# Kernel tuning notes

Hardware: AMD Instinct MI355X
Metric: run time of the kernel (lower is better)

The kernel has to match this reference:

```python
import jax, jax.numpy as jnp
import numpy as np

RADIUS = 4  # matches init radius


def _bilinear_sample(v, grid):
    """Faithful F.grid_sample(v, grid, mode='bilinear', align_corners=True, padding_mode='zeros').
    v: (B,C,H,W); grid: (B,Hg,Wg,2) in [-1,1]; grid[...,0]->width(x), grid[...,1]->height(y)."""
    B, C, H, W = v.shape
    Hg, Wg = grid.shape[1], grid.shape[2]
    ix = (grid[..., 0] + 1.0) * 0.5 * (W - 1)
    iy = (grid[..., 1] + 1.0) * 0.5 * (H - 1)
    x0 = jnp.floor(ix); y0 = jnp.floor(iy)
    x1 = x0 + 1.0;      y1 = y0 + 1.0
    wx1 = ix - x0; wx0 = 1.0 - wx1
    wy1 = iy - y0; wy0 = 1.0 - wy1
    v_flat = v.reshape(B, C, H * W)
    out = jnp.zeros((B, C, Hg, Wg), v.dtype)
    for xf, yf, w in ((x0, y0, wx0 * wy0), (x1, y0, wx1 * wy0),
                      (x0, y1, wx0 * wy1), (x1, y1, wx1 * wy1)):
        valid = (xf >= 0) & (xf <= W - 1) & (yf >= 0) & (yf <= H - 1)
        xi = jnp.clip(xf, 0, W - 1).astype(jnp.int32)
        yi = jnp.clip(yf, 0, H - 1).astype(jnp.int32)
        idx = (yi * W + xi).reshape(B, 1, Hg * Wg)
        g = jnp.take_along_axis(v_flat, idx, axis=2).reshape(B, C, Hg, Wg)
        out = out + g * (w * valid)[:, None, :, :]
    return out


def setup_inputs() -> dict:
    key = jax.random.key(0)
    ks = jax.random.split(key, 5)
    B, C, H, W, K = 4, 128, 128, 128, 8
    x = jax.random.normal(ks[0], (B, C, H, W), jnp.float32)
    psf_tbl = jax.random.randint(ks[1], (B, H, W, K, 2), 0, 128)  # absolute pixel anchors
    delta = jax.random.normal(ks[2], (1, 1, 1, K, 2), jnp.float32) * 0.1
    w_qkv = jax.random.normal(ks[3], (3 * C, C), jnp.float32) * (C ** -0.5)  # 1x1 conv, no bias
    w_proj = jax.random.normal(ks[4], (C, C), jnp.float32) * (C ** -0.5)
    return {"x": x, "psf_tbl": psf_tbl, "delta": delta, "w_qkv": w_qkv, "w_proj": w_proj}


def reference(x, psf_tbl, delta, w_qkv, w_proj):
    B, C, H, W = x.shape
    K = psf_tbl.shape[3]
    qkv = jnp.einsum('oc,bchw->bohw', w_qkv, x)  # 1x1 conv to_qkv
    q, k, v = jnp.split(qkv, 3, axis=1)
    offsets = psf_tbl.astype(x.dtype) + jnp.tanh(delta) * RADIUS  # (B,H,W,K,2)
    norm = jnp.array([H - 1, W - 1], x.dtype)
    grid = (offsets / norm * 2.0 - 1.0).reshape(B, H, W * K, 2)
    k_s = _bilinear_sample(k, grid).reshape(B, C, H, W, K)
    v_s = _bilinear_sample(v, grid).reshape(B, C, H, W, K)
    attn = jnp.einsum('bchw,bchwk->bhwk', q, k_s) * (C ** -0.5)
    attn = jax.nn.softmax(attn, axis=-1)  # softmax over K sampled points
    out = jnp.einsum('bhwk,bchwk->bchw', attn, v_s)
    return x + jnp.einsum('oc,bchw->bohw', w_proj, out)
```

## Files before the change

kernel.cpp:

```cpp
#include <hip/hip_runtime.h>

#define HW 16384
#define C 128

typedef __attribute__((ext_vector_type(8))) short short8;
typedef __attribute__((ext_vector_type(4))) float f32x4;
typedef __attribute__((ext_vector_type(2))) float f32x2;
typedef __attribute__((ext_vector_type(16))) int v16i;

__device__ __forceinline__ unsigned short f2bf(float f) {
  union { float f; unsigned u; } v; v.f = f;
  return (unsigned short)((v.u + 0x7fffu + ((v.u >> 16) & 1u)) >> 16);
}
#if __has_builtin(__builtin_amdgcn_cvt_pk_bf16_f32)
typedef __attribute__((ext_vector_type(2))) __bf16 bf16x2;
__device__ __forceinline__ unsigned pk2(float a, float b) {
  union { bf16x2 v; unsigned u; } cv;
  cv.v = __builtin_amdgcn_cvt_pk_bf16_f32(a, b);
  return cv.u;
}
#else
__device__ __forceinline__ unsigned pk2(float a, float b) {
  return (unsigned)f2bf(a) | ((unsigned)f2bf(b) << 16);
}
#endif
__device__ __forceinline__ unsigned short f2bf1(float a) {
  return (unsigned short)(pk2(a, a) & 0xffffu);
}
__device__ __forceinline__ float bflo(unsigned w) {
  union { unsigned u; float f; } v; v.u = w << 16; return v.f;
}
__device__ __forceinline__ float bfhi(unsigned w) {
  union { unsigned u; float f; } v; v.u = w & 0xffff0000u; return v.f;
}
__device__ __forceinline__ float asf(int u) {
  union { int u; float f; } v; v.u = u; return v.f;
}
__device__ __forceinline__ float bf2f(unsigned short h) {
  union { unsigned u; float f; } v; v.u = ((unsigned)h) << 16; return v.f;
}

__global__ __launch_bounds__(128) void k_prep(const float* __restrict__ w_qkv,
                                              const float* __restrict__ w_proj,
                                              const float* __restrict__ delta,
                                              unsigned short* __restrict__ Mt,
                                              unsigned short* __restrict__ Pm,
                                              float* __restrict__ pw,
                                              int* __restrict__ pi) {
  const int bid = blockIdx.x;
  const int t = threadIdx.x;
  if (bid == 256) {
    if (t < 8) {
      float s0 = tanhf(delta[t * 2 + 0]) * 4.0f;
      float s1 = tanhf(delta[t * 2 + 1]) * 4.0f;
      float f0 = floorf(s0), f1 = floorf(s1);
      pi[2 * t + 0] = (int)f0;
      pi[2 * t + 1] = (int)f1;
      float fx = s0 - f0, fy = s1 - f1;
      pw[4 * t + 0] = (1.0f - fx) * (1.0f - fy);
      pw[4 * t + 1] = fx * (1.0f - fy);
      pw[4 * t + 2] = (1.0f - fx) * fy;
      pw[4 * t + 3] = fx * fy;
    }
    return;
  }
  const int R = bid & 127;
  float acc = 0.0f;
  if (bid < 128) {
    const float* wq = w_qkv;
    const float* wk = w_qkv + 128 * 128;
    #pragma unroll 16
    for (int j = 0; j < 128; ++j)
      acc += wk[j * 128 + R] * wq[j * 128 + t];
    acc *= 0.08838834764831845f;
    Mt[R * 128 + (t ^ ((R & 7) << 3))] = f2bf1(acc);
  } else {
    const float* wv = w_qkv + 2 * 128 * 128;
    const float* wp = w_proj + (size_t)R * 128;
    #pragma unroll 16
    for (int j = 0; j < 128; ++j)
      acc += wp[j] * wv[j * 128 + t];
    Pm[R * 128 + (t ^ ((R & 7) << 3))] = f2bf1(acc);
  }
}

__global__ __launch_bounds__(256) void k_qx(const float* __restrict__ x,
                                            const unsigned short* __restrict__ Mt,
                                            unsigned short* __restrict__ qb,
                                            unsigned* __restrict__ xq) {
  __shared__ __align__(16) unsigned short Xs[128 * 128];
  const int t = threadIdx.x;
  const int gpix0 = blockIdx.x * 128;
  const int b = gpix0 >> 14;
  const int hw0 = gpix0 & (HW - 1);

  const float* xb = x + (size_t)b * C * HW + hw0;
  #pragma unroll
  for (int i = 0; i < 16; ++i) {
    int linear = i * 256 + t;
    int p = linear & 127;
    int c4 = (linear >> 7) * 4;
    float a0 = xb[(size_t)(c4 + 0) * HW + p];
    float a1 = xb[(size_t)(c4 + 1) * HW + p];
    float a2 = xb[(size_t)(c4 + 2) * HW + p];
    float a3 = xb[(size_t)(c4 + 3) * HW + p];
    int cc = c4 ^ ((p & 7) << 3);
    *(uint2*)&Xs[p * 128 + cc] = make_uint2(pk2(a0, a1), pk2(a2, a3));
  }
  __syncthreads();

  #pragma unroll
  for (int i = 0; i < 8; ++i) {
    int linear = i * 256 + t;
    int c8 = (linear & 15) * 8;
    int prow = linear >> 4;
    uint4 v = *(const uint4*)&Xs[prow * 128 + (c8 ^ ((prow & 7) << 3))];
    *(uint4*)&xq[((size_t)(gpix0 + prow)) * 64 + (c8 >> 1)] = v;
  }

  const int wave = t >> 6, lane = t & 63;
  const int wr = wave >> 1, wc = wave & 1;
  const int rsel = lane & 15, quad = lane >> 4;

  f32x4 acc[4][4];
  #pragma unroll
  for (int mi = 0; mi < 4; ++mi)
    #pragma unroll
    for (int ni = 0; ni < 4; ++ni) acc[mi][ni] = (f32x4){0.f, 0.f, 0.f, 0.f};
  #pragma unroll
  for (int ks = 0; ks < 4; ++ks) {
    const int koff = ks * 32 + quad * 8;
    short8 afr[4], bfr[4];
    #pragma unroll
    for (int mi = 0; mi < 4; ++mi) {
      int r = wr * 64 + mi * 16 + rsel;
      afr[mi] = *(const short8*)&Xs[r * 128 + (koff ^ ((r & 7) << 3))];
    }
    #pragma unroll
    for (int ni = 0; ni < 4; ++ni) {
      int r = wc * 64 + ni * 16 + rsel;
      bfr[ni] = *(const short8*)&Mt[r * 128 + (koff ^ ((r & 7) << 3))];
    }
    #pragma unroll
    for (int mi = 0; mi < 4; ++mi)
      #pragma unroll
      for (int ni = 0; ni < 4; ++ni)
        acc[mi][ni] = __builtin_amdgcn_mfma_f32_16x16x32_bf16(afr[mi], bfr[ni], acc[mi][ni], 0, 0, 0);
  }
  __syncthreads();
  #pragma unroll
  for (int mi = 0; mi < 4; ++mi)
    #pragma unroll
    for (int ni = 0; ni < 4; ++ni)
      #pragma unroll
      for (int r = 0; r < 4; ++r) {
        int p = wr * 64 + mi * 16 + quad * 4 + r;
        int ch = wc * 64 + ni * 16 + rsel;
        Xs[p * 128 + (ch ^ ((p & 7) << 3))] = f2bf1(acc[mi][ni][r]);
      }
  __syncthreads();
  #pragma unroll
  for (int i = 0; i < 8; ++i) {
    int linear = i * 256 + t;
    int c8 = (linear & 15) * 8;
    int prow = linear >> 4;
    uint4 v = *(const uint4*)&Xs[prow * 128 + (c8 ^ ((prow & 7) << 3))];
    *(uint4*)(qb + (size_t)(gpix0 + prow) * C + c8) = v;
  }
}

__global__ __launch_bounds__(256) void k_attn(const unsigned short* __restrict__ qb,
                                              const unsigned* __restrict__ xq,
                                              const int* __restrict__ psf,
                                              const int* __restrict__ pwu,
                                              unsigned short* __restrict__ ao) {
  const int t = threadIdx.x;
  const int li = t & 31;
  const int half = (t >> 5) & 1;
  const int gid = blockIdx.x;
  const int b = gid & 3;
  const int grp = gid >> 2;
  const int pixl = (grp << 3) + ((t >> 6) << 1) + half;
  const size_t spix = ((size_t)b << 14) + pixl;

  v16i w0, w1, tpi;
  asm volatile(
      "s_load_dwordx16 %0, %3, 0\n\t"
      "s_load_dwordx16 %1, %3, 64\n\t"
      "s_load_dwordx16 %2, %3, 128\n\t"
      "s_waitcnt lgkmcnt(0)"
      : "=&s"(w0), "=&s"(w1), "=&s"(tpi)
      : "s"(pwu));

  const int4* pr = (const int4*)(psf + spix * 16);
  int4 a0 = pr[0], a1 = pr[1], a2 = pr[2], a3 = pr[3];
  int va[16] = {a0.x, a0.y, a0.z, a0.w, a1.x, a1.y, a1.z, a1.w,
                a2.x, a2.y, a2.z, a2.w, a3.x, a3.y, a3.z, a3.w};

  const uint2 qp = *(const uint2*)((const unsigned*)qb + spix * 64 + 2 * li);
  const float q0 = bflo(qp.x), q1 = bfhi(qp.x);
  const float q2 = bflo(qp.y), q3 = bfhi(qp.y);

  const unsigned* xB = xq + (((size_t)b << 14) << 6);

  float s0[8], s1[8], s2[8], s3[8], dk[8];
  #pragma unroll
  for (int k = 0; k < 8; ++k) {
    const int x0 = va[2 * k + 0] + tpi[2 * k + 0];
    const int y0 = va[2 * k + 1] + tpi[2 * k + 1];
    float t0 = 0.f, t1 = 0.f, t2 = 0.f, t3 = 0.f;
    #pragma unroll
    for (int cn = 0; cn < 4; ++cn) {
      const int xi = x0 + (cn & 1);
      const int yi = y0 + (cn >> 1);
      const bool valid = ((unsigned)xi <= 127u) & ((unsigned)yi <= 127u);
      const int xc = min(max(xi, 0), 127);
      const int yc = min(max(yi, 0), 127);
      const int widx = k * 4 + cn;
      const float wv = valid ? asf(widx < 16 ? w0[widx & 15] : w1[widx & 15]) : 0.0f;
      const uint2 w2 = *(const uint2*)&xB[((size_t)((yc << 7) + xc) << 6) + 2 * li];
      t0 = fmaf(bflo(w2.x), wv, t0); t1 = fmaf(bfhi(w2.x), wv, t1);
      t2 = fmaf(bflo(w2.y), wv, t2); t3 = fmaf(bfhi(w2.y), wv, t3);
    }
    s0[k] = t0; s1[k] = t1; s2[k] = t2; s3[k] = t3;
    dk[k] = fmaf(q0, t0, fmaf(q1, t1, fmaf(q2, t2, q3 * t3)));
  }
  #pragma unroll
  for (int off = 16; off > 0; off >>= 1) {
    #pragma unroll
    for (int k = 0; k < 8; ++k) dk[k] += __shfl_xor(dk[k], off);
  }
  float m = dk[0];
  #pragma unroll
  for (int k = 1; k < 8; ++k) m = fmaxf(m, dk[k]);
  float den = 0.0f;
  #pragma unroll
  for (int k = 0; k < 8; ++k) { dk[k] = __expf(dk[k] - m); den += dk[k]; }
  const float inv = 1.0f / den;
  float o0 = 0.f, o1 = 0.f, o2 = 0.f, o3 = 0.f;
  #pragma unroll
  for (int k = 0; k < 8; ++k) {
    const float pk = dk[k] * inv;
    o0 = fmaf(pk, s0[k], o0); o1 = fmaf(pk, s1[k], o1);
    o2 = fmaf(pk, s2[k], o2); o3 = fmaf(pk, s3[k], o3);
  }
  *(uint2*)((unsigned*)ao + spix * 64 + 2 * li) = make_uint2(pk2(o0, o1), pk2(o2, o3));
}

__global__ __launch_bounds__(256) void k_proj(const unsigned short* __restrict__ ao,
                                              const unsigned short* __restrict__ Pm,
                                              const unsigned short* __restrict__ xqh,
                                              float* __restrict__ out) {
  __shared__ __align__(16) unsigned short As[128 * 128];
  const int t = threadIdx.x;
  const int gpix0 = blockIdx.x * 128;
  const int b = gpix0 >> 14;
  const int hw0 = gpix0 & (HW - 1);

  #pragma unroll
  for (int i = 0; i < 8; ++i) {
    int linear = i * 256 + t;
    int c8 = (linear & 15) * 8;
    int p = linear >> 4;
    uint4 v = *(const uint4*)(ao + (size_t)(gpix0 + p) * C + c8);
    *(uint4*)&As[p * 128 + (c8 ^ ((p & 7) << 3))] = v;
  }
  __syncthreads();

  const int wave = t >> 6, lane = t & 63;
  const int wr = wave >> 1, wc = wave & 1;
  const int rsel = lane & 15, quad = lane >> 4;

  f32x4 acc[4][4];
  #pragma unroll
  for (int mi = 0; mi < 4; ++mi)
    #pragma unroll
    for (int ni = 0; ni < 4; ++ni) acc[mi][ni] = (f32x4){0.f, 0.f, 0.f, 0.f};

  #pragma unroll
  for (int ks = 0; ks < 4; ++ks) {
    const int koff = ks * 32 + quad * 8;
    short8 afr[4], bfr[4];
    #pragma unroll
    for (int mi = 0; mi < 4; ++mi) {
      int r = wr * 64 + mi * 16 + rsel;
      afr[mi] = *(const short8*)&Pm[r * 128 + (koff ^ ((r & 7) << 3))];
    }
    #pragma unroll
    for (int ni = 0; ni < 4; ++ni) {
      int r = wc * 64 + ni * 16 + rsel;
      bfr[ni] = *(const short8*)&As[r * 128 + (koff ^ ((r & 7) << 3))];
    }
    #pragma unroll
    for (int mi = 0; mi < 4; ++mi)
      #pragma unroll
      for (int ni = 0; ni < 4; ++ni)
        acc[mi][ni] = __builtin_amdgcn_mfma_f32_16x16x32_bf16(afr[mi], bfr[ni], acc[mi][ni], 0, 0, 0);
  }

  __syncthreads();
  #pragma unroll
  for (int i = 0; i < 8; ++i) {
    int linear = i * 256 + t;
    int c8 = (linear & 15) * 8;
    int p = linear >> 4;
    uint4 v = *(const uint4*)(xqh + (size_t)(gpix0 + p) * C + c8);
    *(uint4*)&As[p * 128 + (c8 ^ ((p & 7) << 3))] = v;
  }
  __syncthreads();

  #pragma unroll
  for (int mi = 0; mi < 4; ++mi)
    #pragma unroll
    for (int ni = 0; ni < 4; ++ni)
      #pragma unroll
      for (int r = 0; r < 4; ++r) {
        int och = wr * 64 + mi * 16 + quad * 4 + r;
        int pixl = wc * 64 + ni * 16 + rsel;
        float xr = bf2f(As[pixl * 128 + (och ^ ((pixl & 7) << 3))]);
        size_t addr = ((size_t)b * C + och) * HW + hw0 + pixl;
        out[addr] = xr + acc[mi][ni][r];
      }
}

extern "C" void kernel_launch(void* const* d_in, const int* in_sizes, int n_in,
                              void* d_out, int out_size, void* d_ws, size_t ws_size,
                              hipStream_t stream) {
  const float* x      = (const float*)d_in[0];
  const int*   psf    = (const int*)d_in[1];
  const float* delta  = (const float*)d_in[2];
  const float* w_qkv  = (const float*)d_in[3];
  const float* w_proj = (const float*)d_in[4];
  float* out = (float*)d_out;

  const size_t N = (size_t)4 * HW * C;
  unsigned short* qb = (unsigned short*)d_ws;
  unsigned short* xq = qb + N;
  unsigned short* ao = xq + N;
  unsigned short* Mt = ao + N;
  unsigned short* Pm = Mt + 16384;
  float* pw = (float*)(Pm + 16384);
  int*   pi = (int*)(pw + 32);
  (void)pi;

  k_prep<<<dim3(257), 128, 0, stream>>>(w_qkv, w_proj, delta, Mt, Pm, pw, pi);
  k_qx<<<dim3(512), 256, 0, stream>>>(x, Mt, qb, (unsigned*)xq);
  k_attn<<<dim3(8192), 256, 0, stream>>>(qb, (const unsigned*)xq, psf, (const int*)pw, ao);
  k_proj<<<dim3(512), 256, 0, stream>>>(ao, Pm, xq, out);
}
```

Baseline: 149.6 us.

## Split x transpose/convert from q GEMM into separate kernels with more blocks

The fused k_qx kernel is split in two. k_xq converts and transposes x into the bf16 pixel-major buffer using 2048 small blocks with float4 loads. k_q then reads that buffer back and runs the q GEMM. The aim is more parallelism and better coalescing for the memory-bound transpose, at the cost of an extra launch and a re-read of xq. The gather offset in k_attn is also switched to 32-bit unsigned arithmetic to cut address computation.

```diff
diff --git a/kernel.cpp b/kernel.cpp
--- a/kernel.cpp
+++ b/kernel.cpp
@@ -84,39 +84,54 @@
   }
 }
 
-__global__ __launch_bounds__(256) void k_qx(const float* __restrict__ x,
-                                            const unsigned short* __restrict__ Mt,
-                                            unsigned short* __restrict__ qb,
+__global__ __launch_bounds__(256) void k_xq(const float* __restrict__ x,
                                             unsigned* __restrict__ xq) {
-  __shared__ __align__(16) unsigned short Xs[128 * 128];
-  const int t = threadIdx.x;
-  const int gpix0 = blockIdx.x * 128;
+  __shared__ __align__(16) unsigned short Xs[32 * 128];
+  const int t = threadIdx.x;
+  const int gpix0 = blockIdx.x * 32;
   const int b = gpix0 >> 14;
   const int hw0 = gpix0 & (HW - 1);
-
   const float* xb = x + (size_t)b * C * HW + hw0;
-  #pragma unroll
-  for (int i = 0; i < 16; ++i) {
-    int linear = i * 256 + t;
-    int p = linear & 127;
-    int c4 = (linear >> 7) * 4;
-    float a0 = xb[(size_t)(c4 + 0) * HW + p];
-    float a1 = xb[(size_t)(c4 + 1) * HW + p];
-    float a2 = xb[(size_t)(c4 + 2) * HW + p];
-    float a3 = xb[(size_t)(c4 + 3) * HW + p];
-    int cc = c4 ^ ((p & 7) << 3);
-    *(uint2*)&Xs[p * 128 + cc] = make_uint2(pk2(a0, a1), pk2(a2, a3));
-  }
-  __syncthreads();
+
+  #pragma unroll
+  for (int i = 0; i < 4; ++i) {
+    int idx = i * 256 + t;
+    int c = idx >> 3;
+    int p4 = idx & 7;
+    float4 v = *(const float4*)(xb + (size_t)c * HW + p4 * 4);
+    int p0 = p4 * 4;
+    Xs[(p0 + 0) * 128 + (c ^ (((p0 + 0) & 7) << 3))] = f2bf1(v.x);
+    Xs[(p0 + 1) * 128 + (c ^ (((p0 + 1) & 7) << 3))] = f2bf1(v.y);
+    Xs[(p0 + 2) * 128 + (c ^ (((p0 + 2) & 7) << 3))] = f2bf1(v.z);
+    Xs[(p0 + 3) * 128 + (c ^ (((p0 + 3) & 7) << 3))] = f2bf1(v.w);
+  }
+  __syncthreads();
+  #pragma unroll
+  for (int i = 0; i < 2; ++i) {
+    int idx = i * 256 + t;
+    int pix = idx >> 4;
+    int c8 = (idx & 15) * 8;
+    uint4 v = *(const uint4*)&Xs[pix * 128 + (c8 ^ ((pix & 7) << 3))];
+    *(uint4*)&xq[(size_t)(gpix0 + pix) * 64 + (c8 >> 1)] = v;
+  }
+}
+
+__global__ __launch_bounds__(256) void k_q(const unsigned short* __restrict__ xqh,
+                                           const unsigned short* __restrict__ Mt,
+                                           unsigned short* __restrict__ qb) {
+  __shared__ __align__(16) unsigned short Xs[128 * 128];
+  const int t = threadIdx.x;
+  const int gpix0 = blockIdx.x * 128;
 
   #pragma unroll
   for (int i = 0; i < 8; ++i) {
     int linear = i * 256 + t;
     int c8 = (linear & 15) * 8;
-    int prow = linear >> 4;
-    uint4 v = *(const uint4*)&Xs[prow * 128 + (c8 ^ ((prow & 7) << 3))];
-    *(uint4*)&xq[((size_t)(gpix0 + prow)) * 64 + (c8 >> 1)] = v;
-  }
+    int p = linear >> 4;
+    uint4 v = *(const uint4*)(xqh + (size_t)(gpix0 + p) * C + c8);
+    *(uint4*)&Xs[p * 128 + (c8 ^ ((p & 7) << 3))] = v;
+  }
+  __syncthreads();
 
   const int wave = t >> 6, lane = t & 63;
   const int wr = wave >> 1, wc = wave & 1;
@@ -218,7 +233,8 @@
       const int yc = min(max(yi, 0), 127);
       const int widx = k * 4 + cn;
       const float wv = valid ? asf(widx < 16 ? w0[widx & 15] : w1[widx & 15]) : 0.0f;
-      const uint2 w2 = *(const uint2*)&xB[((size_t)((yc << 7) + xc) << 6) + 2 * li];
+      const unsigned off = (((unsigned)((yc << 7) + xc)) << 6) + 2u * (unsigned)li;
+      const uint2 w2 = *(const uint2*)&xB[off];
       t0 = fmaf(bflo(w2.x), wv, t0); t1 = fmaf(bfhi(w2.x), wv, t1);
       t2 = fmaf(bflo(w2.y), wv, t2); t3 = fmaf(bfhi(w2.y), wv, t3);
     }
@@ -344,7 +360,8 @@
   (void)pi;
 
   k_prep<<<dim3(257), 128, 0, stream>>>(w_qkv, w_proj, delta, Mt, Pm, pw, pi);
-  k_qx<<<dim3(512), 256, 0, stream>>>(x, Mt, qb, (unsigned*)xq);
+  k_xq<<<dim3(2048), 256, 0, stream>>>(x, (unsigned*)xq);
+  k_q<<<dim3(512), 256, 0, stream>>>(xq, Mt, qb);
   k_attn<<<dim3(8192), 256, 0, stream>>>(qb, (const unsigned*)xq, psf, (const int*)pw, ao);
   k_proj<<<dim3(512), 256, 0, stream>>>(ao, Pm, xq, out);
 }
```

After: 155.9 us. 4.2% more time.

## Fuse output projection and residual add into attention kernel

Applied to the files above, without the earlier changes.

Folds the separate projection GEMM kernel into the attention kernel. Each 8-pixel block stages its bf16 attention output in LDS, padded to 16 rows, and runs a small MFMA against the projection weights. It then adds the fp32 residual from x and writes the result directly. This removes the ao round-trip through global memory and one kernel launch. In exchange, each block reads the whole 32KB Pm matrix for only 8 pixels, half the MFMA work is wasted on padding, and the output stores are only 8 floats contiguous per channel row. The gather address math is also narrowed to 32-bit offsets.

```diff
diff --git a/kernel.cpp b/kernel.cpp
--- a/kernel.cpp
+++ b/kernel.cpp
@@ -35,9 +35,6 @@
 }
 __device__ __forceinline__ float asf(int u) {
   union { int u; float f; } v; v.u = u; return v.f;
-}
-__device__ __forceinline__ float bf2f(unsigned short h) {
-  union { unsigned u; float f; } v; v.u = ((unsigned)h) << 16; return v.f;
 }
 
 __global__ __launch_bounds__(128) void k_prep(const float* __restrict__ w_qkv,
@@ -173,15 +170,22 @@
                                               const unsigned* __restrict__ xq,
                                               const int* __restrict__ psf,
                                               const int* __restrict__ pwu,
-                                              unsigned short* __restrict__ ao) {
+                                              const unsigned short* __restrict__ Pm,
+                                              const float* __restrict__ x,
+                                              float* __restrict__ out) {
+  __shared__ __align__(16) unsigned short Ot[16 * 128];
   const int t = threadIdx.x;
   const int li = t & 31;
   const int half = (t >> 5) & 1;
+  const int wave = t >> 6;
   const int gid = blockIdx.x;
   const int b = gid & 3;
   const int grp = gid >> 2;
-  const int pixl = (grp << 3) + ((t >> 6) << 1) + half;
+  const int p0 = grp << 3;
+  const int pixl = p0 + (wave << 1) + half;
   const size_t spix = ((size_t)b << 14) + pixl;
+
+  ((uint2*)(Ot + 8 * 128))[t] = make_uint2(0u, 0u);
 
   v16i w0, w1, tpi;
   asm volatile(
@@ -218,7 +222,8 @@
       const int yc = min(max(yi, 0), 127);
       const int widx = k * 4 + cn;
       const float wv = valid ? asf(widx < 16 ? w0[widx & 15] : w1[widx & 15]) : 0.0f;
-      const uint2 w2 = *(const uint2*)&xB[((size_t)((yc << 7) + xc) << 6) + 2 * li];
+      const unsigned off = (((unsigned)((yc << 7) + xc)) << 6) + 2u * (unsigned)li;
+      const uint2 w2 = *(const uint2*)&xB[off];
       t0 = fmaf(bflo(w2.x), wv, t0); t1 = fmaf(bfhi(w2.x), wv, t1);
       t2 = fmaf(bflo(w2.y), wv, t2); t3 = fmaf(bfhi(w2.y), wv, t3);
     }
@@ -244,83 +249,38 @@
     o0 = fmaf(pk, s0[k], o0); o1 = fmaf(pk, s1[k], o1);
     o2 = fmaf(pk, s2[k], o2); o3 = fmaf(pk, s3[k], o3);
   }
-  *(uint2*)((unsigned*)ao + spix * 64 + 2 * li) = make_uint2(pk2(o0, o1), pk2(o2, o3));
-}
-
-__global__ __launch_bounds__(256) void k_proj(const unsigned short* __restrict__ ao,
-                                              const unsigned short* __restrict__ Pm,
-                                              const unsigned short* __restrict__ xqh,
-                                              float* __restrict__ out) {
-  __shared__ __align__(16) unsigned short As[128 * 128];
-  const int t = threadIdx.x;
-  const int gpix0 = blockIdx.x * 128;
-  const int b = gpix0 >> 14;
-  const int hw0 = gpix0 & (HW - 1);
-
-  #pragma unroll
-  for (int i = 0; i < 8; ++i) {
-    int linear = i * 256 + t;
-    int c8 = (linear & 15) * 8;
-    int p = linear >> 4;
-    uint4 v = *(const uint4*)(ao + (size_t)(gpix0 + p) * C + c8);
-    *(uint4*)&As[p * 128 + (c8 ^ ((p & 7) << 3))] = v;
-  }
+  const int prow = (wave << 1) + half;
+  *(uint2*)&Ot[prow * 128 + ((4 * li) ^ ((prow & 7) << 3))] =
+      make_uint2(pk2(o0, o1), pk2(o2, o3));
   __syncthreads();
 
-  const int wave = t >> 6, lane = t & 63;
-  const int wr = wave >> 1, wc = wave & 1;
-  const int rsel = lane & 15, quad = lane >> 4;
-
-  f32x4 acc[4][4];
-  #pragma unroll
-  for (int mi = 0; mi < 4; ++mi)
-    #pragma unroll
-    for (int ni = 0; ni < 4; ++ni) acc[mi][ni] = (f32x4){0.f, 0.f, 0.f, 0.f};
-
-  #pragma unroll
-  for (int ks = 0; ks < 4; ++ks) {
-    const int koff = ks * 32 + quad * 8;
-    short8 afr[4], bfr[4];
-    #pragma unroll
-    for (int mi = 0; mi < 4; ++mi) {
-      int r = wr * 64 + mi * 16 + rsel;
-      afr[mi] = *(const short8*)&Pm[r * 128 + (koff ^ ((r & 7) << 3))];
-    }
-    #pragma unroll
-    for (int ni = 0; ni < 4; ++ni) {
-      int r = wc * 64 + ni * 16 + rsel;
-      bfr[ni] = *(const short8*)&As[r * 128 + (koff ^ ((r & 7) << 3))];
-    }
-    #pragma unroll
-    for (int mi = 0; mi < 4; ++mi)
-      #pragma unroll
-      for (int ni = 0; ni < 4; ++ni)
-        acc[mi][ni] = __builtin_amdgcn_mfma_f32_16x16x32_bf16(afr[mi], bfr[ni], acc[mi][ni], 0, 0, 0);
-  }
-
-  __syncthreads();
-  #pragma unroll
-  for (int i = 0; i < 8; ++i) {
-    int linear = i * 256 + t;
-    int c8 = (linear & 15) * 8;
-    int p = linear >> 4;
-    uint4 v = *(const uint4*)(xqh + (size_t)(gpix0 + p) * C + c8);
-    *(uint4*)&As[p * 128 + (c8 ^ ((p & 7) << 3))] = v;
-  }
-  __syncthreads();
-
-  #pragma unroll
-  for (int mi = 0; mi < 4; ++mi)
-    #pragma unroll
-    for (int ni = 0; ni < 4; ++ni)
+  {
+    const int rsel = t & 15, quad = (t >> 4) & 3;
+    f32x4 pa0 = (f32x4){0.f, 0.f, 0.f, 0.f};
+    f32x4 pa1 = (f32x4){0.f, 0.f, 0.f, 0.f};
+    #pragma unroll
+    for (int ks = 0; ks < 4; ++ks) {
+      const int koff = ks * 32 + quad * 8;
+      short8 bfr = *(const short8*)&Ot[rsel * 128 + (koff ^ ((rsel & 7) << 3))];
+      int r0 = wave * 32 + rsel;
+      short8 af0 = *(const short8*)&Pm[r0 * 128 + (koff ^ ((r0 & 7) << 3))];
+      int r1 = wave * 32 + 16 + rsel;
+      short8 af1 = *(const short8*)&Pm[r1 * 128 + (koff ^ ((r1 & 7) << 3))];
+      pa0 = __builtin_amdgcn_mfma_f32_16x16x32_bf16(af0, bfr, pa0, 0, 0, 0);
+      pa1 = __builtin_amdgcn_mfma_f32_16x16x32_bf16(af1, bfr, pa1, 0, 0, 0);
+    }
+    if (rsel < 8) {
       #pragma unroll
       for (int r = 0; r < 4; ++r) {
-        int och = wr * 64 + mi * 16 + quad * 4 + r;
-        int pixl = wc * 64 + ni * 16 + rsel;
-        float xr = bf2f(As[pixl * 128 + (och ^ ((pixl & 7) << 3))]);
-        size_t addr = ((size_t)b * C + och) * HW + hw0 + pixl;
-        out[addr] = xr + acc[mi][ni][r];
+        int och0 = wave * 32 + quad * 4 + r;
+        size_t ad0 = ((size_t)b * C + och0) * HW + p0 + rsel;
+        out[ad0] = x[ad0] + pa0[r];
+        int och1 = och0 + 16;
+        size_t ad1 = ((size_t)b * C + och1) * HW + p0 + rsel;
+        out[ad1] = x[ad1] + pa1[r];
       }
+    }
+  }
 }
 
 extern "C" void kernel_launch(void* const* d_in, const int* in_sizes, int n_in,
@@ -336,8 +296,7 @@
   const size_t N = (size_t)4 * HW * C;
   unsigned short* qb = (unsigned short*)d_ws;
   unsigned short* xq = qb + N;
-  unsigned short* ao = xq + N;
-  unsigned short* Mt = ao + N;
+  unsigned short* Mt = xq + N;
   unsigned short* Pm = Mt + 16384;
   float* pw = (float*)(Pm + 16384);
   int*   pi = (int*)(pw + 32);
@@ -345,6 +304,6 @@
 
   k_prep<<<dim3(257), 128, 0, stream>>>(w_qkv, w_proj, delta, Mt, Pm, pw, pi);
   k_qx<<<dim3(512), 256, 0, stream>>>(x, Mt, qb, (unsigned*)xq);
-  k_attn<<<dim3(8192), 256, 0, stream>>>(qb, (const unsigned*)xq, psf, (const int*)pw, ao);
-  k_proj<<<dim3(512), 256, 0, stream>>>(ao, Pm, xq, out);
-}
+  k_attn<<<dim3(8192), 256, 0, stream>>>(qb, (const unsigned*)xq, psf, (const int*)pw,
+                                         Pm, x, out);
+}
```

Result: slower. 165.7 us (+10.7%).
